# Performance work log

Hardware: AMD Instinct MI355X
Metric: run time of the kernel (lower is better)

## Reference

```python
import jax, jax.numpy as jnp
import numpy as np

D_MODEL = 1024
N_HEADS = 16
D_HEAD = D_MODEL // N_HEADS
D_FF = 4096
B, T = 2, 2048


def setup_inputs() -> dict:
    key = jax.random.key(0)
    ks = jax.random.split(key, 8)
    s = 0.02
    return {
        "x": jax.random.normal(ks[0], (B, T, D_MODEL), dtype=jnp.float32),
        "wq": jax.random.normal(ks[1], (D_MODEL, D_MODEL), dtype=jnp.float32) * s,
        "wk": jax.random.normal(ks[2], (D_MODEL, D_MODEL), dtype=jnp.float32) * s,
        "wv": jax.random.normal(ks[3], (D_MODEL, D_MODEL), dtype=jnp.float32) * s,
        "wo": jax.random.normal(ks[4], (D_MODEL, D_MODEL), dtype=jnp.float32) * s,
        "w1": jax.random.normal(ks[5], (D_FF, D_MODEL), dtype=jnp.float32) * s,
        "b1": jnp.zeros((D_FF,), dtype=jnp.float32),
        "w2": jax.random.normal(ks[6], (D_MODEL, D_FF), dtype=jnp.float32) * s,
        "b2": jnp.zeros((D_MODEL,), dtype=jnp.float32),
        "ln1_g": jnp.ones((D_MODEL,), dtype=jnp.float32),
        "ln1_b": jnp.zeros((D_MODEL,), dtype=jnp.float32),
        "ln2_g": jnp.ones((D_MODEL,), dtype=jnp.float32),
        "ln2_b": jnp.zeros((D_MODEL,), dtype=jnp.float32),
    }


def _layernorm(x, g, b, eps=1e-5):
    mu = jnp.mean(x, axis=-1, keepdims=True)
    var = jnp.mean(jnp.square(x - mu), axis=-1, keepdims=True)
    return (x - mu) * jax.lax.rsqrt(var + eps) * g + b


def reference(x, wq, wk, wv, wo, w1, b1, w2, b2, ln1_g, ln1_b, ln2_g, ln2_b):
    Bsz, Tlen, C = x.shape
    h = _layernorm(x, ln1_g, ln1_b)
    # torch Linear: y = h @ W^T ; reshape to [B, H, T, Dh]
    def proj(w):
        return (h @ w.T).reshape(Bsz, Tlen, N_HEADS, D_HEAD).transpose(0, 2, 1, 3)
    q, k, v = proj(wq), proj(wk), proj(wv)
    scores = jnp.einsum('bhqd,bhkd->bhqk', q, k) / np.sqrt(D_HEAD).astype(np.float32)
    p = jax.nn.softmax(scores.astype(jnp.float32), axis=-1).astype(scores.dtype)
    out = jnp.einsum('bhqk,bhkd->bhqd', p, v)
    out = out.transpose(0, 2, 1, 3).reshape(Bsz, Tlen, C)
    x = x + out @ wo.T
    h2 = _layernorm(x, ln2_g, ln2_b)
    ff = jax.nn.gelu(h2 @ w1.T + b1, approximate=False) @ w2.T + b2
    return x + ff
```

## Files before the change

kernel.cpp:

```cpp
#include <hip/hip_runtime.h>
#include <hip/hip_bf16.h>
#include <math.h>

#define DM   1024
#define NH   16
#define DH   64
#define DFF  4096
#define BB   2
#define TT   2048
#define MTOK (BB*TT)
#define QS   3072

typedef unsigned short u16;
typedef unsigned int   u32;
typedef __attribute__((ext_vector_type(8))) __bf16 bf16x8;
typedef __attribute__((ext_vector_type(4))) float  f32x4;

__device__ inline float bf2f(u16 u) { return __uint_as_float(((u32)u) << 16); }
__device__ inline u16 f2bf(float f) {
  u32 u = __float_as_uint(f);
  u += 0x7FFFu + ((u >> 16) & 1u);
  return (u16)(u >> 16);
}
__device__ inline u32 packtrunc(float lo, float hi) {
  return __builtin_amdgcn_perm(__float_as_uint(hi), __float_as_uint(lo), 0x07060302u);
}
__device__ inline float fexp2(float x) { return __builtin_amdgcn_exp2f(x); }

__device__ inline void gload_lds16(const void* g, void* l) {
  __builtin_amdgcn_global_load_lds(
      (const __attribute__((address_space(1))) void*)g,
      (__attribute__((address_space(3))) void*)l,
      16, 0, 0);
}

__global__ __launch_bounds__(256) void prep(
    const float* __restrict__ wq, const float* __restrict__ wk, const float* __restrict__ wv,
    const float* __restrict__ wo, const float* __restrict__ w1, const float* __restrict__ w2,
    const float* __restrict__ x, const float* __restrict__ g, const float* __restrict__ be,
    u16* __restrict__ wqkv_b, u16* __restrict__ wo_b, u16* __restrict__ w1_b,
    u16* __restrict__ w2_b, u16* __restrict__ h1)
{
  const int blk = blockIdx.x;
  if (blk < 12288) {
    const float* src; u16* dst; int idx;
    if (blk < 3072) {
      idx = blk * 256 + threadIdx.x;
      const int sel = idx >> 18;
      const int j = idx & 0x3FFFF;
      src = sel == 0 ? wq : (sel == 1 ? wk : wv);
      dst = wqkv_b;
      float4 v = ((const float4*)src)[j];
      ushort4 o; o.x = f2bf(v.x); o.y = f2bf(v.y); o.z = f2bf(v.z); o.w = f2bf(v.w);
      ((ushort4*)dst)[idx] = o;
      return;
    } else if (blk < 4096) { src = wo; dst = wo_b; idx = (blk - 3072) * 256 + threadIdx.x; }
    else if (blk < 8192)   { src = w1; dst = w1_b; idx = (blk - 4096) * 256 + threadIdx.x; }
    else                   { src = w2; dst = w2_b; idx = (blk - 8192) * 256 + threadIdx.x; }
    float4 v = ((const float4*)src)[idx];
    ushort4 o; o.x = f2bf(v.x); o.y = f2bf(v.y); o.z = f2bf(v.z); o.w = f2bf(v.w);
    ((ushort4*)dst)[idx] = o;
    return;
  }
  const int w = threadIdx.x >> 6, lane = threadIdx.x & 63;
  const int row = (blk - 12288) * 4 + w;
  const float4* xr = (const float4*)(x + (size_t)row * DM);
  float4 v[4];
  float s = 0.f, s2 = 0.f;
#pragma unroll
  for (int i = 0; i < 4; i++) {
    v[i] = xr[i * 64 + lane];
    s  += v[i].x + v[i].y + v[i].z + v[i].w;
    s2 += v[i].x * v[i].x + v[i].y * v[i].y + v[i].z * v[i].z + v[i].w * v[i].w;
  }
#pragma unroll
  for (int off = 32; off > 0; off >>= 1) {
    s  += __shfl_xor(s,  off);
    s2 += __shfl_xor(s2, off);
  }
  const float mu = s * (1.f / DM);
  const float rs = rsqrtf(s2 * (1.f / DM) - mu * mu + 1e-5f);
  u16* orow = h1 + (size_t)row * DM;
#pragma unroll
  for (int i = 0; i < 4; i++) {
    const float4 gg = ((const float4*)g)[i * 64 + lane];
    const float4 bb = ((const float4*)be)[i * 64 + lane];
    ushort4 o;
    o.x = f2bf((v[i].x - mu) * rs * gg.x + bb.x);
    o.y = f2bf((v[i].y - mu) * rs * gg.y + bb.y);
    o.z = f2bf((v[i].z - mu) * rs * gg.z + bb.z);
    o.w = f2bf((v[i].w - mu) * rs * gg.w + bb.w);
    ((ushort4*)orow)[i * 64 + lane] = o;
  }
}

__global__ __launch_bounds__(256) void reduce_ln(
    const float* __restrict__ x, const float* __restrict__ P,
    const float* __restrict__ g, const float* __restrict__ be,
    float* __restrict__ xmid, u16* __restrict__ h2)
{
  const float* P0 = P;
  const float* P1 = P + (size_t)MTOK * DM;
  const int w = threadIdx.x >> 6, lane = threadIdx.x & 63;
  const int row = blockIdx.x * 4 + w;
  const size_t roff = (size_t)row * DM;
  float4 v[4];
  float s = 0.f, s2 = 0.f;
#pragma unroll
  for (int i = 0; i < 4; i++) {
    const float4 a = ((const float4*)(x  + roff))[i * 64 + lane];
    const float4 p = ((const float4*)(P0 + roff))[i * 64 + lane];
    const float4 qv = ((const float4*)(P1 + roff))[i * 64 + lane];
    v[i].x = a.x + p.x + qv.x; v[i].y = a.y + p.y + qv.y;
    v[i].z = a.z + p.z + qv.z; v[i].w = a.w + p.w + qv.w;
    ((float4*)(xmid + roff))[i * 64 + lane] = v[i];
    s  += v[i].x + v[i].y + v[i].z + v[i].w;
    s2 += v[i].x * v[i].x + v[i].y * v[i].y + v[i].z * v[i].z + v[i].w * v[i].w;
  }
#pragma unroll
  for (int off = 32; off > 0; off >>= 1) {
    s  += __shfl_xor(s,  off);
    s2 += __shfl_xor(s2, off);
  }
  const float mu = s * (1.f / DM);
  const float rs = rsqrtf(s2 * (1.f / DM) - mu * mu + 1e-5f);
  u16* orow = h2 + roff;
#pragma unroll
  for (int i = 0; i < 4; i++) {
    const float4 gg = ((const float4*)g)[i * 64 + lane];
    const float4 bb = ((const float4*)be)[i * 64 + lane];
    ushort4 o;
    o.x = f2bf((v[i].x - mu) * rs * gg.x + bb.x);
    o.y = f2bf((v[i].y - mu) * rs * gg.y + bb.y);
    o.z = f2bf((v[i].z - mu) * rs * gg.z + bb.z);
    o.w = f2bf((v[i].w - mu) * rs * gg.w + bb.w);
    ((ushort4*)orow)[i * 64 + lane] = o;
  }
}

__global__ __launch_bounds__(256) void reduce_out(
    const float* __restrict__ Q, const float* __restrict__ xmid,
    const float* __restrict__ b2, float* __restrict__ out)
{
  const float* Q0 = Q;
  const float* Q1 = Q + (size_t)MTOK * DM;
  const int i = blockIdx.x * 256 + threadIdx.x;
  const float4 a = ((const float4*)xmid)[i];
  const float4 p = ((const float4*)Q0)[i];
  const float4 qv = ((const float4*)Q1)[i];
  const float4 bb = ((const float4*)b2)[i & (DM / 4 - 1)];
  float4 o;
  o.x = a.x + p.x + qv.x + bb.x; o.y = a.y + p.y + qv.y + bb.y;
  o.z = a.z + p.z + qv.z + bb.z; o.w = a.w + p.w + qv.w + bb.w;
  ((float4*)out)[i] = o;
}

template <int EPI, int BN>
__global__ __launch_bounds__(256) void gemm_bt(
    const u16* __restrict__ A, const u16* __restrict__ Bw,
    int M, int N, int K,
    const float* __restrict__ bias,
    u16* __restrict__ outB, float oscale, int scaleN)
{
  constexpr int NJ = BN / 32;
  __shared__ u16 As[128 * 64];
  __shared__ u16 Bs[BN * 64];

  const int tid  = threadIdx.x;
  const int w    = tid >> 6;
  const int lane = tid & 63;
  const int wr   = w >> 1, wc = w & 1;
  const int q    = lane >> 4;
  const int li   = lane & 15;
  const int rowBase = blockIdx.y * 128;
  const int colBase = blockIdx.x * BN;

  const int lr = lane >> 3;
  const int cs = (lane & 7) ^ lr;
  const u16* Abase = A  + (size_t)(rowBase + lr) * K + cs * 8;
  const u16* Bbase = Bw + (size_t)(colBase + lr) * K + cs * 8;

  f32x4 acc[4][NJ] = {};

  for (int k0 = 0; k0 < K; k0 += 64) {
    __syncthreads();
#pragma unroll
    for (int jj = 0; jj < 4; jj++) {
      const int rb = (w * 4 + jj) * 8;
      gload_lds16(Abase + (size_t)rb * K + k0, &As[rb * 64]);
    }
#pragma unroll
    for (int jj = 0; jj < NJ; jj++) {
      const int rb = (w * NJ + jj) * 8;
      gload_lds16(Bbase + (size_t)rb * K + k0, &Bs[rb * 64]);
    }
    __syncthreads();
#pragma unroll
    for (int kk = 0; kk < 2; kk++) {
      bf16x8 fa[4], fb[NJ];
      const int pos = (kk * 4 + q) ^ (li & 7);
#pragma unroll
      for (int i = 0; i < 4; i++) {
        const int row = wr * 64 + i * 16 + li;
        fa[i] = *(const bf16x8*)&As[row * 64 + pos * 8];
      }
#pragma unroll
      for (int j = 0; j < NJ; j++) {
        const int row = wc * (BN / 2) + j * 16 + li;
        fb[j] = *(const bf16x8*)&Bs[row * 64 + pos * 8];
      }
#pragma unroll
      for (int i = 0; i < 4; i++)
#pragma unroll
        for (int j = 0; j < NJ; j++)
          acc[i][j] = __builtin_amdgcn_mfma_f32_16x16x32_bf16(fa[i], fb[j], acc[i][j], 0, 0, 0);
    }
  }

#pragma unroll
  for (int i = 0; i < 4; i++) {
#pragma unroll
    for (int j = 0; j < NJ; j++) {
      const int col = colBase + wc * (BN / 2) + j * 16 + li;
      float bv = 0.f;
      if constexpr (EPI == 2) bv = bias[col];
#pragma unroll
      for (int r = 0; r < 4; r++) {
        const int row = rowBase + wr * 64 + i * 16 + q * 4 + r;
        float v = acc[i][j][r] + bv;
        if constexpr (EPI == 2) {
          const float z = fexp2(-v * (2.302213f + 0.1029625f * v * v));
          v = v * __builtin_amdgcn_rcpf(1.f + z);
        }
        if constexpr (EPI == 0) {
          const float sc = (col < scaleN) ? oscale : 1.f;
          v *= sc;
        }
        outB[(size_t)row * N + col] = f2bf(v);
      }
    }
  }
}

__global__ __launch_bounds__(256) void gemm_sk(
    const u16* __restrict__ A, const u16* __restrict__ Bw,
    int N, int K, int KLEN, float* __restrict__ P)
{
  __shared__ u16 As[128 * 64];
  __shared__ u16 Bs[64 * 64];

  const int tid  = threadIdx.x;
  const int w    = tid >> 6;
  const int lane = tid & 63;
  const int wr   = w >> 1, wc = w & 1;
  const int q    = lane >> 4;
  const int li   = lane & 15;
  const int rowBase = blockIdx.y * 128;
  const int colBase = blockIdx.x * 64;
  const int koff = blockIdx.z * KLEN;

  const int lr = lane >> 3;
  const int cs = (lane & 7) ^ lr;
  const u16* Abase = A  + (size_t)(rowBase + lr) * K + koff + cs * 8;
  const u16* Bbase = Bw + (size_t)(colBase + lr) * K + koff + cs * 8;

  f32x4 acc[4][2] = {};

  for (int k0 = 0; k0 < KLEN; k0 += 64) {
    __syncthreads();
#pragma unroll
    for (int jj = 0; jj < 4; jj++) {
      const int rb = (w * 4 + jj) * 8;
      gload_lds16(Abase + (size_t)rb * K + k0, &As[rb * 64]);
    }
#pragma unroll
    for (int jj = 0; jj < 2; jj++) {
      const int rb = (w * 2 + jj) * 8;
      gload_lds16(Bbase + (size_t)rb * K + k0, &Bs[rb * 64]);
    }
    __syncthreads();
#pragma unroll
    for (int kk = 0; kk < 2; kk++) {
      bf16x8 fa[4], fb[2];
      const int pos = (kk * 4 + q) ^ (li & 7);
#pragma unroll
      for (int i = 0; i < 4; i++) {
        const int row = wr * 64 + i * 16 + li;
        fa[i] = *(const bf16x8*)&As[row * 64 + pos * 8];
      }
#pragma unroll
      for (int j = 0; j < 2; j++) {
        const int row = wc * 32 + j * 16 + li;
        fb[j] = *(const bf16x8*)&Bs[row * 64 + pos * 8];
      }
#pragma unroll
      for (int i = 0; i < 4; i++)
#pragma unroll
        for (int j = 0; j < 2; j++)
          acc[i][j] = __builtin_amdgcn_mfma_f32_16x16x32_bf16(fa[i], fb[j], acc[i][j], 0, 0, 0);
    }
  }

  float* Pz = P + (size_t)blockIdx.z * MTOK * DM;
#pragma unroll
  for (int i = 0; i < 4; i++)
#pragma unroll
    for (int j = 0; j < 2; j++) {
      const int col = colBase + wc * 32 + j * 16 + li;
#pragma unroll
      for (int r = 0; r < 4; r++) {
        const int row = rowBase + wr * 64 + i * 16 + q * 4 + r;
        Pz[(size_t)row * N + col] = acc[i][j][r];
      }
    }
}

__global__ __launch_bounds__(256) void transpose_v(
    const u16* __restrict__ vq, u16* __restrict__ vt)
{
  __shared__ u16 t[64][72];
  const int bh = blockIdx.x, b = bh >> 4, h = bh & 15;
  const int t0 = blockIdx.y * 64;
  const int tid = threadIdx.x;
  const int r = tid >> 2, c = (tid & 3) * 16;
  const u16* src = vq + (size_t)(b * TT + t0 + r) * QS + h * DH + c;
#pragma unroll
  for (int i = 0; i < 4; i++)
    *(ushort4*)&t[r][c + i * 4] = ((const ushort4*)src)[i];
  __syncthreads();
  const int dh = tid >> 2, tt = (tid & 3) * 16;
  u16* dst = vt + ((size_t)bh * 64 + dh) * TT + t0 + tt;
#pragma unroll
  for (int i = 0; i < 4; i++) {
    ushort4 o;
    o.x = t[tt + i * 4 + 0][dh]; o.y = t[tt + i * 4 + 1][dh];
    o.z = t[tt + i * 4 + 2][dh]; o.w = t[tt + i * 4 + 3][dh];
    ((ushort4*)dst)[i] = o;
  }
}

__global__ __launch_bounds__(512) void attn_mfma(
    const u16* __restrict__ qb, const u16* __restrict__ kb,
    const u16* __restrict__ vt, u16* __restrict__ ob)
{
  __shared__ u16 Ks[2][64 * 64];
  __shared__ u16 Vs[2][64 * 64];
  __shared__ u16 Sh[8 * 16 * 72];

  const int tid = threadIdx.x, w = tid >> 6, lane = tid & 63;
  const int q = lane >> 4, li = lane & 15;
  const int bh = blockIdx.x, b = bh >> 4, h = bh & 15;
  const int q0 = blockIdx.y * 128;
  const int lr8 = lane >> 3, lc8 = lane & 7;

#pragma unroll
  for (int jj = 0; jj < 2; jj++) {
    const int rb = w * 16 + jj * 8;
    const int row = rb + lr8;
    const int cs = lc8 ^ (row & 7);
    gload_lds16(qb + (size_t)(b * TT + q0 + row) * QS + h * DH + cs * 8,
                &Sh[rb * 64]);
  }
  __syncthreads();

  bf16x8 qf[2];
#pragma unroll
  for (int kk = 0; kk < 2; kk++) {
    const int row = w * 16 + li;
    const int pos = (kk * 4 + q) ^ (li & 7);
    qf[kk] = *(const bf16x8*)&Sh[row * 64 + pos * 8];
  }

  auto stage = [&](int buf, int kt) {
    const int rb = w * 8;
    const int row = rb + lr8;
    const int cs = lc8 ^ (row & 7);
    gload_lds16(kb + (size_t)(b * TT + kt + row) * QS + h * DH + cs * 8,
                &Ks[buf][rb * 64]);
    gload_lds16(vt + ((size_t)bh * 64 + row) * TT + kt + cs * 8,
                &Vs[buf][rb * 64]);
  };

  f32x4 ot[4] = {};
  float lsum = 0.f;
  u16* Pw = &Sh[w * 16 * 72];

  stage(0, 0);
  for (int it = 0; it < TT / 64; it++) {
    __syncthreads();
    if (it + 1 < TT / 64) stage((it + 1) & 1, (it + 1) * 64);
    const u16* Kc = Ks[it & 1];
    const u16* Vc = Vs[it & 1];

    f32x4 st[4] = {};
#pragma unroll
    for (int kk = 0; kk < 2; kk++)
#pragma unroll
      for (int i = 0; i < 4; i++) {
        const int pos = (kk * 4 + q) ^ (li & 7);
        const bf16x8 kf = *(const bf16x8*)&Kc[(i * 16 + li) * 64 + pos * 8];
        st[i] = __builtin_amdgcn_mfma_f32_16x16x32_bf16(kf, qf[kk], st[i], 0, 0, 0);
      }

    u32 pk[4][2];
#pragma unroll
    for (int i = 0; i < 4; i++) {
      const float p0 = fexp2(st[i][0]);
      const float p1 = fexp2(st[i][1]);
      const float p2 = fexp2(st[i][2]);
      const float p3 = fexp2(st[i][3]);
      lsum += (p0 + p1) + (p2 + p3);
      pk[i][0] = packtrunc(p0, p1);
      pk[i][1] = packtrunc(p2, p3);
    }

#pragma unroll
    for (int i = 0; i < 4; i++) {
      const int a = li * 72 + i * 16 + q * 4;
      *(u32*)&Pw[a]     = pk[i][0];
      *(u32*)&Pw[a + 2] = pk[i][1];
    }

#pragma unroll
    for (int kk = 0; kk < 2; kk++) {
      const bf16x8 pf = *(const bf16x8*)&Pw[li * 72 + kk * 32 + q * 8];
#pragma unroll
      for (int m = 0; m < 4; m++) {
        const int pos = (kk * 4 + q) ^ (li & 7);
        const bf16x8 vf = *(const bf16x8*)&Vc[(m * 16 + li) * 64 + pos * 8];
        ot[m] = __builtin_amdgcn_mfma_f32_16x16x32_bf16(vf, pf, ot[m], 0, 0, 0);
      }
    }
  }

  float s = lsum;
  s += __shfl_xor(s, 16);
  s += __shfl_xor(s, 32);
  const float inv = 1.f / s;
#pragma unroll
  for (int m = 0; m < 4; m++) {
    const int a = li * 72 + m * 16 + q * 4;
    *(u32*)&Pw[a]     = packtrunc(ot[m][0] * inv, ot[m][1] * inv);
    *(u32*)&Pw[a + 2] = packtrunc(ot[m][2] * inv, ot[m][3] * inv);
  }
#pragma unroll
  for (int pass = 0; pass < 2; pass++) {
    const int row = pass * 8 + lr8;
    const bf16x8 v = *(const bf16x8*)&Pw[row * 72 + lc8 * 8];
    const int token = q0 + w * 16 + row;
    *(bf16x8*)(ob + ((size_t)(b * TT + token) * NH + h) * DH + lc8 * 8) = v;
  }
}

extern "C" void kernel_launch(void* const* d_in, const int* in_sizes, int n_in,
                              void* d_out, int out_size, void* d_ws, size_t ws_size,
                              hipStream_t stream) {
  const float* x    = (const float*)d_in[0];
  const float* wq   = (const float*)d_in[1];
  const float* wk   = (const float*)d_in[2];
  const float* wv   = (const float*)d_in[3];
  const float* wo   = (const float*)d_in[4];
  const float* w1   = (const float*)d_in[5];
  const float* b1   = (const float*)d_in[6];
  const float* w2   = (const float*)d_in[7];
  const float* b2   = (const float*)d_in[8];
  const float* ln1g = (const float*)d_in[9];
  const float* ln1b = (const float*)d_in[10];
  const float* ln2g = (const float*)d_in[11];
  const float* ln2b = (const float*)d_in[12];

  size_t off = 0;
  char* base = (char*)d_ws;
  auto alloc = [&](size_t bytes) { void* p = base + off; off += bytes; return p; };

  u16* wqkv_b = (u16*)alloc((size_t)3 * DM * DM * 2);
  u16* wo_b   = (u16*)alloc((size_t)DM * DM * 2);
  u16* w1_b   = (u16*)alloc((size_t)DFF * DM * 2);
  u16* w2_b   = (u16*)alloc((size_t)DM * DFF * 2);
  u16* h1     = (u16*)alloc((size_t)MTOK * DM * 2);
  u16* qkvb   = (u16*)alloc((size_t)MTOK * QS * 2);
  u16* attn   = (u16*)alloc((size_t)MTOK * DM * 2);
  u16* h2     = (u16*)alloc((size_t)MTOK * DM * 2);
  u16* ff1    = (u16*)alloc((size_t)MTOK * DFF * 2);
  float* xmid = (float*)alloc((size_t)MTOK * DM * 4);
  u16* vtb    = ff1;
  float* woP  = (float*)ff1;
  float* ff2P = (float*)h1;
  (void)ws_size; (void)in_sizes; (void)n_in; (void)out_size;

  prep<<<13312, 256, 0, stream>>>(wq, wk, wv, wo, w1, w2, x, ln1g, ln1b,
                                  wqkv_b, wo_b, w1_b, w2_b, h1);

  const float QSCALE = 0.125f * 1.44269504088896340736f;
  gemm_bt<0, 128><<<dim3(QS / 128, MTOK / 128), 256, 0, stream>>>(
      h1, wqkv_b, MTOK, QS, DM, nullptr, qkvb, QSCALE, DM);

  transpose_v<<<dim3(BB * NH, TT / 64), 256, 0, stream>>>(qkvb + 2 * DM, vtb);
  attn_mfma<<<dim3(BB * NH, TT / 128), 512, 0, stream>>>(qkvb, qkvb + DM, vtb, attn);

  gemm_sk<<<dim3(DM / 64, MTOK / 128, 2), 256, 0, stream>>>(
      attn, wo_b, DM, DM, DM / 2, woP);
  reduce_ln<<<MTOK / 4, 256, 0, stream>>>(x, woP, ln2g, ln2b, xmid, h2);

  gemm_bt<2, 128><<<dim3(DFF / 128, MTOK / 128), 256, 0, stream>>>(
      h2, w1_b, MTOK, DFF, DM, b1, ff1, 1.f, 0);
  gemm_sk<<<dim3(DM / 64, MTOK / 128, 2), 256, 0, stream>>>(
      ff1, w2_b, DM, DFF, DFF / 2, ff2P);
  reduce_out<<<MTOK * DM / 4 / 256, 256, 0, stream>>>(ff2P, xmid, b2, (float*)d_out);
}
```

Measured before the change: 343.0 us.

## Add 256x256-tile triple-buffered GEMM for FFN1 with swizzled block order

Adds a new GEMM kernel with 256x256 output tiles, 512 threads and a three-stage LDS ring fed by direct global-to-LDS loads. It also remaps blocks across XCDs and swizzles LDS chunks to avoid bank conflicts. The kernel replaces the 128-tile GEMM for the first FFN projection with fused bias+GELU, aiming for higher arithmetic intensity and better load/compute overlap. The grid is only 16x16 blocks, and the large accumulator array may pressure registers and limit occupancy.

```diff
diff --git a/kernel.cpp b/kernel.cpp
--- a/kernel.cpp
+++ b/kernel.cpp
@@ -242,6 +242,101 @@
   }
 }
 
+template <int EPI>
+__global__ __launch_bounds__(512, 2) void gemm256(
+    const u16* __restrict__ A, const u16* __restrict__ Bw,
+    int M, int N, int K,
+    const float* __restrict__ bias,
+    u16* __restrict__ outB, float oscale, int scaleN)
+{
+  __shared__ u16 lds[3 * 16384];
+
+  const int tid  = threadIdx.x;
+  const int w    = tid >> 6;
+  const int lane = tid & 63;
+  const int wr   = w >> 2, wc = w & 3;
+  const int q    = lane >> 4, li = lane & 15;
+
+  const int nbx = gridDim.x, nwg = nbx * gridDim.y;
+  int bid = blockIdx.y * nbx + blockIdx.x;
+  bid = (bid & 7) * (nwg >> 3) + (bid >> 3);
+  const int bx = bid % nbx, by = bid / nbx;
+  const int rowBase = by * 256, colBase = bx * 256;
+
+  const int srow = lane >> 2;
+  const int schk = (lane & 3) ^ ((lane >> 3) & 3);
+  const u16* Asrc = A  + (size_t)(rowBase + srow) * K + schk * 8;
+  const u16* Bsrc = Bw + (size_t)(colBase + srow) * K + schk * 8;
+  const int wbase = w * 16;
+
+  auto stage = [&](int kt, int bsel) {
+    const int k0 = kt * 32;
+    u16* bb = &lds[bsel * 16384];
+#pragma unroll
+    for (int half = 0; half < 2; half++) {
+      const int rb = half * 128 + wbase;
+      gload_lds16(Asrc + (size_t)rb * K + k0, &bb[rb * 32]);
+      gload_lds16(Bsrc + (size_t)rb * K + k0, &bb[8192 + rb * 32]);
+    }
+  };
+
+  f32x4 acc[8][4] = {};
+  const int NT = K >> 5;
+  const int pos = q ^ ((li >> 1) & 3);
+
+  stage(0, 0);
+  stage(1, 1);
+
+  int csel = 0, ssel = 2;
+  for (int kt = 0; kt < NT; ++kt) {
+    if (kt < NT - 1) asm volatile("s_waitcnt vmcnt(4)" ::: "memory");
+    else             asm volatile("s_waitcnt vmcnt(0)" ::: "memory");
+    __builtin_amdgcn_s_barrier();
+    const u16* bb = &lds[csel * 16384];
+    bf16x8 fa[8], fb[4];
+#pragma unroll
+    for (int m = 0; m < 8; m++)
+      fa[m] = *(const bf16x8*)&bb[(wr * 128 + m * 16 + li) * 32 + pos * 8];
+#pragma unroll
+    for (int n = 0; n < 4; n++)
+      fb[n] = *(const bf16x8*)&bb[8192 + (wc * 64 + n * 16 + li) * 32 + pos * 8];
+    if (kt + 2 < NT) stage(kt + 2, ssel);
+    __builtin_amdgcn_s_setprio(1);
+#pragma unroll
+    for (int m = 0; m < 8; m++)
+#pragma unroll
+      for (int n = 0; n < 4; n++)
+        acc[m][n] = __builtin_amdgcn_mfma_f32_16x16x32_bf16(fa[m], fb[n], acc[m][n], 0, 0, 0);
+    __builtin_amdgcn_s_setprio(0);
+    csel = (csel == 2) ? 0 : csel + 1;
+    ssel = (ssel == 2) ? 0 : ssel + 1;
+  }
+
+#pragma unroll
+  for (int n = 0; n < 4; n++) {
+    const int col = colBase + wc * 64 + n * 16 + li;
+    float bv = 0.f;
+    if constexpr (EPI == 2) bv = bias[col];
+#pragma unroll
+    for (int m = 0; m < 8; m++) {
+#pragma unroll
+      for (int r = 0; r < 4; r++) {
+        const int row = rowBase + wr * 128 + m * 16 + q * 4 + r;
+        float v = acc[m][n][r] + bv;
+        if constexpr (EPI == 2) {
+          const float z = fexp2(-v * (2.302213f + 0.1029625f * v * v));
+          v = v * __builtin_amdgcn_rcpf(1.f + z);
+        }
+        if constexpr (EPI == 0) {
+          const float sc = (col < scaleN) ? oscale : 1.f;
+          v *= sc;
+        }
+        outB[(size_t)row * N + col] = f2bf(v);
+      }
+    }
+  }
+}
+
 __global__ __launch_bounds__(256) void gemm_sk(
     const u16* __restrict__ A, const u16* __restrict__ Bw,
     int N, int K, int KLEN, float* __restrict__ P)
@@ -502,7 +597,7 @@
       attn, wo_b, DM, DM, DM / 2, woP);
   reduce_ln<<<MTOK / 4, 256, 0, stream>>>(x, woP, ln2g, ln2b, xmid, h2);
 
-  gemm_bt<2, 128><<<dim3(DFF / 128, MTOK / 128), 256, 0, stream>>>(
+  gemm256<2><<<dim3(DFF / 256, MTOK / 256), 512, 0, stream>>>(
       h2, w1_b, MTOK, DFF, DM, b1, ff1, 1.f, 0);
   gemm_sk<<<dim3(DM / 64, MTOK / 128, 2), 256, 0, stream>>>(
       ff1, w2_b, DM, DFF, DFF / 2, ff2P);
```

Result: no change. 337.0 us (-1.8%).
